# Kernel optimization log

Measured on AMD Instinct MI355X. Metric: run time of the kernel, lower is better.

## Reference

```python
import jax, jax.numpy as jnp
import numpy as np

D_MODEL = 1024
D_STATE = 16
D_CONV = 3
EXPAND = 2
MLP_RATIO = 4
HEADDIM = 64
D_INNER = EXPAND * D_MODEL            # 2048
NHEADS = D_INNER // HEADDIM           # 32
CONV_DIM = D_INNER + 2 * D_STATE      # x, B, C all go through the depthwise conv
D_IN_PROJ = 2 * D_INNER + 2 * D_STATE + NHEADS


def rmsnorm(x, w, eps=1e-6):
    return x * jax.lax.rsqrt(jnp.mean(x * x, axis=-1, keepdims=True) + eps) * w


def silu(x):
    return x * jax.nn.sigmoid(x)


def causal_depthwise_conv(x, w, b):
    # x: (B, L, C); w: (C, K); b: (C,)  -- causal depthwise conv over L
    B, L, C = x.shape
    K = w.shape[1]
    xp = jnp.pad(x, ((0, 0), (K - 1, 0), (0, 0)))
    out = b
    for k in range(K):  # tiny fixed loop over kernel taps (K=3)
        out = out + w[:, k] * xp[:, k:k + L, :]
    return out


def mamba2(h, W_in, conv_w, conv_b, dt_bias, A_log, D, norm_gate_w, W_out):
    B, L, _ = h.shape
    zxbcdt = h @ W_in  # (B, L, D_IN_PROJ)
    z = zxbcdt[..., :D_INNER]
    xBC = zxbcdt[..., D_INNER:D_INNER + CONV_DIM]
    dt = jax.nn.softplus(zxbcdt[..., D_INNER + CONV_DIM:] + dt_bias)  # (B, L, H)

    xBC = silu(causal_depthwise_conv(xBC, conv_w, conv_b))
    x = xBC[..., :D_INNER].reshape(B, L, NHEADS, HEADDIM)
    Bmat = xBC[..., D_INNER:D_INNER + D_STATE]   # (B, L, N)
    Cmat = xBC[..., D_INNER + D_STATE:]          # (B, L, N)

    A = -jnp.exp(A_log)                          # (H,)
    dA = jnp.exp(dt * A)                         # (B, L, H)
    dBx = jnp.einsum('blhp,bln,blh->blhpn', x, Bmat, dt)  # (B, L, H, P, N)

    def step(state, inp):
        dA_t, dBx_t = inp                        # (B,H), (B,H,P,N)
        state = state * dA_t[:, :, None, None] + dBx_t
        return state, state

    s0 = jnp.zeros((B, NHEADS, HEADDIM, D_STATE), dtype=h.dtype)
    _, states = jax.lax.scan(step, s0,
                             (jnp.moveaxis(dA, 1, 0), jnp.moveaxis(dBx, 1, 0)))
    # states: (L, B, H, P, N)
    y = jnp.einsum('lbhpn,bln->blhp', states, Cmat)
    y = y + D[None, None, :, None] * x
    y = y.reshape(B, L, D_INNER)
    y = rmsnorm(y * silu(z), norm_gate_w, eps=1e-5)  # gated RMSNorm as in Mamba2
    return y @ W_out


def setup_inputs() -> dict:
    key = jax.random.key(0)
    ks = jax.random.split(key, 12)
    f = jnp.float32
    d = {}
    d['x'] = jax.random.normal(ks[0], (2, 2048, D_MODEL), dtype=f)
    d['norm1_w'] = jnp.ones((D_MODEL,), f)
    d['W_in'] = jax.random.normal(ks[1], (D_MODEL, D_IN_PROJ), f) * (D_MODEL ** -0.5)
    d['conv_w'] = jax.random.normal(ks[2], (CONV_DIM, D_CONV), f) * 0.2
    d['conv_b'] = jnp.zeros((CONV_DIM,), f)
    d['dt_bias'] = jnp.log(jnp.expm1(jax.random.uniform(ks[3], (NHEADS,), f, 0.001, 0.1)))
    d['A_log'] = jnp.log(jax.random.uniform(ks[4], (NHEADS,), f, 1.0, 16.0))
    d['D'] = jnp.ones((NHEADS,), f)
    d['norm_gate_w'] = jnp.ones((D_INNER,), f)
    d['W_out'] = jax.random.normal(ks[5], (D_INNER, D_MODEL), f) * (D_INNER ** -0.5)
    d['norm2_w'] = jnp.ones((D_MODEL,), f)
    d['mlp_w1'] = jax.random.normal(ks[6], (D_MODEL, D_MODEL * MLP_RATIO), f) * (D_MODEL ** -0.5)
    d['mlp_b1'] = jnp.zeros((D_MODEL * MLP_RATIO,), f)
    d['mlp_w2'] = jax.random.normal(ks[7], (D_MODEL * MLP_RATIO, D_MODEL), f) * ((D_MODEL * MLP_RATIO) ** -0.5)
    d['mlp_b2'] = jnp.zeros((D_MODEL,), f)
    return d


def reference(x, norm1_w, W_in, conv_w, conv_b, dt_bias, A_log, D,
              norm_gate_w, W_out, norm2_w, mlp_w1, mlp_b1, mlp_w2, mlp_b2):
    h = rmsnorm(x, norm1_w)
    h = mamba2(h, W_in, conv_w, conv_b, dt_bias, A_log, D, norm_gate_w, W_out)
    x = x + h
    h = rmsnorm(x, norm2_w)
    h = silu(h @ mlp_w1 + mlp_b1) @ mlp_w2 + mlp_b2
    return x + h
```

## Files before the change

kernel.cpp:

```cpp
#include <hip/hip_runtime.h>

typedef __bf16 bf16;
typedef __bf16 bf16x4 __attribute__((ext_vector_type(4)));
typedef __bf16 bf16x8 __attribute__((ext_vector_type(8)));
typedef float  f32x4  __attribute__((ext_vector_type(4)));

#define BATCH  2
#define SEQ    2048
#define ROWS   (BATCH*SEQ)
#define DMODEL 1024
#define DINNER 2048
#define DSTATE 16
#define NH     32
#define HD     64
#define CONVD  2080
#define DPROJ  4160
#define DMLP   4096
#define DTOFF  (DINNER + CONVD)
#define CS     64
#define NCHUNK (SEQ/CS)

__device__ __forceinline__ float sigmoidf_(float x) { return 1.f / (1.f + expf(-x)); }

__device__ __forceinline__ float blockSum256(float v) {
    #pragma unroll
    for (int o = 32; o > 0; o >>= 1) v += __shfl_down(v, o);
    __shared__ float sb[4];
    const int tid = threadIdx.x;
    if ((tid & 63) == 0) sb[tid >> 6] = v;
    __syncthreads();
    return sb[0] + sb[1] + sb[2] + sb[3];
}

__device__ __forceinline__ void gload_lds16(const bf16* g, bf16* l) {
    __builtin_amdgcn_global_load_lds((const __attribute__((address_space(1))) void*)g,
                                     (__attribute__((address_space(3))) void*)l, 16, 0, 0);
}

__device__ __forceinline__ int xcd_swz(int orig, int nwg) {
    const int q = nwg >> 3, r = nwg & 7;
    const int x = orig & 7, i = orig >> 3;
    return (x < r ? x * (q + 1) : r * (q + 1) + (x - r) * q) + i;
}

__global__ __launch_bounds__(256) void transpose_k(const float* __restrict__ in,
                                                   bf16* __restrict__ out, int R, int C) {
    __shared__ float t[32][33];
    const int bx = blockIdx.x * 32, by = blockIdx.y * 32;
    const int tx = threadIdx.x, ty = threadIdx.y;
    #pragma unroll
    for (int i = 0; i < 4; ++i)
        t[ty + i * 8][tx] = in[(size_t)(by + ty + i * 8) * C + bx + tx];
    __syncthreads();
    #pragma unroll
    for (int i = 0; i < 4; ++i)
        out[(size_t)(bx + ty + i * 8) * R + by + tx] = (bf16)t[tx][ty + i * 8];
}

template<int EPI>
__global__ __launch_bounds__(512) void gemm256_k(
    const bf16* __restrict__ A, const bf16* __restrict__ BT,
    int K, int ldN, int colofs, int nbx, int nby,
    bf16* __restrict__ outb, float* __restrict__ outf,
    const float* __restrict__ bias, size_t pstride)
{
    __shared__ __align__(16) bf16 As[2][256 * 64];
    __shared__ __align__(16) bf16 Bs[2][256 * 64];
    const int nwg = (int)gridDim.x;
    const int wg  = xcd_swz((int)blockIdx.x, nwg);
    const int bx  = wg % nbx;
    const int t2  = wg / nbx;
    const int by  = t2 % nby;
    const int sl  = t2 / nby;
    const int ns  = nwg / (nbx * nby);
    const int Ks  = K / ns;
    const int kbeg = sl * Ks;

    const int tid  = threadIdx.x;
    const int lane = tid & 63, wid = tid >> 6;
    const int wm = wid >> 2, wn = wid & 3;
    const int lr = lane & 15, lk = lane >> 4;
    const int X  = lr & 7;
    const int brow = by * 256, bcol = bx * 256;

    size_t aoff[4], boff[4];
    #pragma unroll
    for (int i = 0; i < 4; ++i) {
        const int g = tid + i * 512;
        const int srow = g >> 3;
        const int scol = ((g & 7) ^ (srow & 7)) * 8;
        aoff[i] = (size_t)(brow + srow) * K + scol;
        boff[i] = (size_t)(bcol + srow) * K + scol;
    }

    auto stage = [&](int buf, int k0) {
        #pragma unroll
        for (int i = 0; i < 4; ++i)
            gload_lds16(A + aoff[i] + k0, As[buf] + (tid + i * 512) * 8);
        #pragma unroll
        for (int i = 0; i < 4; ++i)
            gload_lds16(BT + boff[i] + k0, Bs[buf] + (tid + i * 512) * 8);
    };

    f32x4 acc[8][4] = {};
    const int nt = Ks >> 6;
    stage(0, kbeg);
    __syncthreads();
    for (int t = 0; t < nt; ++t) {
        const int cur = t & 1;
        if (t + 1 < nt) stage(cur ^ 1, kbeg + (t + 1) * 64);
        #pragma unroll
        for (int kk = 0; kk < 2; ++kk) {
            const int off = ((kk * 4 + lk) ^ X) * 8;
            bf16x8 bfr[4];
            #pragma unroll
            for (int n = 0; n < 4; ++n)
                bfr[n] = *(const bf16x8*)(Bs[cur] + (wn * 64 + n * 16 + lr) * 64 + off);
            #pragma unroll
            for (int m = 0; m < 8; ++m) {
                const bf16x8 af = *(const bf16x8*)(As[cur] + (wm * 128 + m * 16 + lr) * 64 + off);
                #pragma unroll
                for (int n = 0; n < 4; ++n)
                    acc[m][n] = __builtin_amdgcn_mfma_f32_16x16x32_bf16(af, bfr[n], acc[m][n], 0, 0, 0);
            }
        }
        __syncthreads();
    }

    #pragma unroll
    for (int m = 0; m < 8; ++m) {
        const int grow = brow + wm * 128 + m * 16 + lk * 4;
        #pragma unroll
        for (int n = 0; n < 4; ++n) {
            const int gcol = colofs + bcol + wn * 64 + n * 16 + lr;
            #pragma unroll
            for (int j = 0; j < 4; ++j) {
                const int row = grow + j;
                float v = acc[m][n][j];
                if constexpr (EPI == 0) {
                    outb[(size_t)row * ldN + gcol] = (bf16)v;
                } else if constexpr (EPI == 1) {
                    v += bias[gcol];
                    outb[(size_t)row * ldN + gcol] = (bf16)(v * sigmoidf_(v));
                } else {
                    outf[pstride * sl + (size_t)row * ldN + gcol] = v;
                }
            }
        }
    }
}

template<int EPI>
__global__ __launch_bounds__(256) void gemm_bt(
    const bf16* __restrict__ A, const bf16* __restrict__ BT,
    int M, int N, int K, int nbx, int nby, int ldN, int colofs,
    bf16* __restrict__ outb, float* __restrict__ dtout)
{
    __shared__ __align__(16) bf16 As[2][128 * 64];
    __shared__ __align__(16) bf16 Bs[2][128 * 64];
    const int nwg = (int)gridDim.x;
    const int wg  = xcd_swz((int)blockIdx.x, nwg);
    const int bx  = wg % nbx;
    const int by  = (wg / nbx) % nby;

    const int tid  = threadIdx.x;
    const int brow = by * 128;
    const int bcol = bx * 128;
    const int lane = tid & 63;
    const int wid  = tid >> 6;
    const int wm = wid >> 1, wn = wid & 1;
    const int lr = lane & 15, lk = lane >> 4;
    const int X  = lr & 7;
    const int off0 = ((lk) ^ X) * 8;
    const int off1 = ((4 + lk) ^ X) * 8;

    f32x4 acc[4][4] = {};

    size_t aoff[4], boff[4];
    #pragma unroll
    for (int i = 0; i < 4; ++i) {
        const int g = tid + i * 256;
        const int srow = g >> 3;
        const int scol = ((g & 7) ^ (srow & 7)) * 8;
        aoff[i] = (size_t)(brow + srow) * K + scol;
        int bn = bcol + srow; if (bn > N - 1) bn = N - 1;
        boff[i] = (size_t)bn * K + scol;
    }

    auto stage = [&](int buf, int k0) {
        #pragma unroll
        for (int i = 0; i < 4; ++i)
            gload_lds16(A + aoff[i] + k0, As[buf] + (tid + i * 256) * 8);
        #pragma unroll
        for (int i = 0; i < 4; ++i)
            gload_lds16(BT + boff[i] + k0, Bs[buf] + (tid + i * 256) * 8);
    };

    const int nt = K >> 6;
    stage(0, 0);
    __syncthreads();
    for (int t = 0; t < nt; ++t) {
        const int cur = t & 1;
        if (t + 1 < nt) stage(cur ^ 1, (t + 1) * 64);
        #pragma unroll
        for (int kk = 0; kk < 2; ++kk) {
            const int off = kk ? off1 : off0;
            bf16x8 af[4], bfr[4];
            #pragma unroll
            for (int m = 0; m < 4; ++m)
                af[m] = *(const bf16x8*)(As[cur] + (wm * 64 + m * 16 + lr) * 64 + off);
            #pragma unroll
            for (int n = 0; n < 4; ++n)
                bfr[n] = *(const bf16x8*)(Bs[cur] + (wn * 64 + n * 16 + lr) * 64 + off);
            #pragma unroll
            for (int m = 0; m < 4; ++m)
                #pragma unroll
                for (int n = 0; n < 4; ++n)
                    acc[m][n] = __builtin_amdgcn_mfma_f32_16x16x32_bf16(af[m], bfr[n], acc[m][n], 0, 0, 0);
        }
        __syncthreads();
    }

    #pragma unroll
    for (int m = 0; m < 4; ++m) {
        const int grow = brow + wm * 64 + m * 16 + lk * 4;
        #pragma unroll
        for (int n = 0; n < 4; ++n) {
            const int gcol = bcol + wn * 64 + n * 16 + lr;
            if (gcol >= N) continue;
            #pragma unroll
            for (int j = 0; j < 4; ++j) {
                const int row = grow + j;
                const float v = acc[m][n][j];
                const int gc = colofs + gcol;
                outb[(size_t)row * ldN + gc] = (bf16)v;
                if (gc >= DTOFF)
                    dtout[(size_t)row * NH + (gc - DTOFF)] = v;
            }
        }
    }
}

template<int WITH_BIAS>
__global__ __launch_bounds__(256) void reduce_k(const float* __restrict__ part,
                                                const float* __restrict__ res,
                                                const float* __restrict__ bias,
                                                float* __restrict__ out, int MN) {
    const int i = (blockIdx.x * 256 + threadIdx.x) * 4;
    if (i >= MN) return;
    const float4 a = *(const float4*)(part + i);
    const float4 b = *(const float4*)(part + (size_t)MN + i);
    const float4 c = *(const float4*)(part + 2 * (size_t)MN + i);
    const float4 d = *(const float4*)(part + 3 * (size_t)MN + i);
    const float4 r = *(const float4*)(res + i);
    float4 o;
    o.x = a.x + b.x + c.x + d.x + r.x;
    o.y = a.y + b.y + c.y + d.y + r.y;
    o.z = a.z + b.z + c.z + d.z + r.z;
    o.w = a.w + b.w + c.w + d.w + r.w;
    if constexpr (WITH_BIAS) {
        const int col = i & (DMODEL - 1);
        o.x += bias[col]; o.y += bias[col + 1]; o.z += bias[col + 2]; o.w += bias[col + 3];
    }
    *(float4*)(out + i) = o;
}

__global__ __launch_bounds__(256) void rmsnorm_k(const float* __restrict__ in,
                                                 const float* __restrict__ w,
                                                 bf16* __restrict__ out, float eps) {
    const int row = blockIdx.x, tid = threadIdx.x;
    const float4 v = *(const float4*)(in + (size_t)row * DMODEL + tid * 4);
    float f[4] = { v.x, v.y, v.z, v.w };
    float ss = f[0]*f[0] + f[1]*f[1] + f[2]*f[2] + f[3]*f[3];
    ss = blockSum256(ss);
    const float scale = rsqrtf(ss * (1.f / DMODEL) + eps);
    const float4 wv = *(const float4*)(w + tid * 4);
    const float wa[4] = { wv.x, wv.y, wv.z, wv.w };
    bf16x4 o;
    #pragma unroll
    for (int j = 0; j < 4; ++j) o[j] = (bf16)(f[j] * scale * wa[j]);
    *(bf16x4*)(out + (size_t)row * DMODEL + tid * 4) = o;
}

__global__ __launch_bounds__(256) void rmsgate_k(const float* __restrict__ y,
                                                 const bf16* __restrict__ zx,
                                                 const float* __restrict__ w,
                                                 bf16* __restrict__ out) {
    const int row = blockIdx.x, tid = threadIdx.x;
    const float* yr = y + (size_t)row * DINNER;
    const bf16*  zr = zx + (size_t)row * DPROJ;
    float vals[8];
    float ss = 0.f;
    #pragma unroll
    for (int i = 0; i < 2; ++i) {
        const float4 yv = *(const float4*)(yr + tid * 8 + i * 4);
        const bf16x4 zv = *(const bf16x4*)(zr + tid * 8 + i * 4);
        const float ya[4] = { yv.x, yv.y, yv.z, yv.w };
        #pragma unroll
        for (int j = 0; j < 4; ++j) {
            const float z = (float)zv[j];
            const float t = ya[j] * (z * sigmoidf_(z));
            vals[i * 4 + j] = t;
            ss += t * t;
        }
    }
    ss = blockSum256(ss);
    const float scale = rsqrtf(ss * (1.f / DINNER) + 1e-5f);
    bf16* orow = out + (size_t)row * DINNER + tid * 8;
    #pragma unroll
    for (int i = 0; i < 2; ++i) {
        bf16x4 o;
        #pragma unroll
        for (int j = 0; j < 4; ++j)
            o[j] = (bf16)(vals[i * 4 + j] * scale * w[tid * 8 + i * 4 + j]);
        *(bf16x4*)(orow + i * 4) = o;
    }
}

__global__ __launch_bounds__(256) void conv_silu_k(const bf16* __restrict__ zx,
                                                   const float* __restrict__ cw,
                                                   const float* __restrict__ cb,
                                                   float* __restrict__ xBC) {
    const int idx = blockIdx.x * 256 + threadIdx.x;
    if (idx >= ROWS * CONVD) return;
    const int c  = idx % CONVD;
    const int bl = idx / CONVD;
    const int l  = bl % SEQ;
    float acc = cb[c];
    const bf16* col = zx + (size_t)bl * DPROJ + DINNER + c;
    if (l >= 2) acc += cw[c * 3 + 0] * (float)col[-2 * DPROJ];
    if (l >= 1) acc += cw[c * 3 + 1] * (float)col[-1 * DPROJ];
    acc += cw[c * 3 + 2] * (float)col[0];
    acc = acc * sigmoidf_(acc);
    xBC[(size_t)bl * CONVD + c] = acc;
}

__global__ __launch_bounds__(256) void dtda_k(const float* __restrict__ dtraw,
                                              const float* __restrict__ dt_bias,
                                              const float* __restrict__ A_log,
                                              float* __restrict__ dtb,
                                              float* __restrict__ dab) {
    const int idx = blockIdx.x * 256 + threadIdx.x;
    if (idx >= ROWS * NH) return;
    const int h = idx & (NH - 1);
    const float raw = dtraw[idx] + dt_bias[h];
    const float dt = raw > 20.f ? raw : log1pf(expf(raw));
    const float dA = expf(-expf(A_log[h]) * dt);
    dtb[idx] = dt;
    dab[idx] = dA;
}

__global__ __launch_bounds__(256) void scan1_k(const float* __restrict__ xBC,
                                               const float* __restrict__ dtb,
                                               const float* __restrict__ dab,
                                               float* __restrict__ Sloc,
                                               float* __restrict__ Pc) {
    const int c = blockIdx.x & (NCHUNK - 1);
    const int h = (blockIdx.x >> 5) & (NH - 1);
    const int b = blockIdx.x >> 10;
    const int tid = threadIdx.x;
    const int p  = tid >> 2;
    const int nq = (tid & 3) * 4;
    const size_t rb = (size_t)b * SEQ + c * CS;
    const float* xrow = xBC + rb * CONVD + h * HD + p;
    const float* Brow = xBC + rb * CONVD + DINNER + nq;
    const float* dtp = dtb + rb * NH + h;
    const float* dap = dab + rb * NH + h;
    float s0 = 0.f, s1 = 0.f, s2 = 0.f, s3 = 0.f, P = 1.f;
    for (int l = 0; l < CS; ++l) {
        const float xv  = xrow[(size_t)l * CONVD];
        const float4 Bv = *(const float4*)(Brow + (size_t)l * CONVD);
        const float dtv = dtp[l * NH];
        const float dav = dap[l * NH];
        const float xdt = xv * dtv;
        s0 = s0 * dav + xdt * Bv.x;
        s1 = s1 * dav + xdt * Bv.y;
        s2 = s2 * dav + xdt * Bv.z;
        s3 = s3 * dav + xdt * Bv.w;
        P *= dav;
    }
    float4* dst = (float4*)(Sloc + (size_t)blockIdx.x * 1024 + tid * 4);
    *dst = make_float4(s0, s1, s2, s3);
    if (tid == 0) Pc[blockIdx.x] = P;
}

__global__ __launch_bounds__(256) void scan2_k(const float* __restrict__ Sloc,
                                               const float* __restrict__ Pc,
                                               float* __restrict__ Sini) {
    const int bh = blockIdx.x;
    const int tid = threadIdx.x;
    const size_t base = (size_t)bh * NCHUNK;
    float c0 = 0.f, c1 = 0.f, c2 = 0.f, c3 = 0.f;
    for (int c = 0; c < NCHUNK; ++c) {
        *(float4*)(Sini + (base + c) * 1024 + tid * 4) = make_float4(c0, c1, c2, c3);
        const float4 sl = *(const float4*)(Sloc + (base + c) * 1024 + tid * 4);
        const float P = Pc[base + c];
        c0 = c0 * P + sl.x;
        c1 = c1 * P + sl.y;
        c2 = c2 * P + sl.z;
        c3 = c3 * P + sl.w;
    }
}

__global__ __launch_bounds__(256) void scan3_k(const float* __restrict__ xBC,
                                               const float* __restrict__ dtb,
                                               const float* __restrict__ dab,
                                               const float* __restrict__ Dp,
                                               const float* __restrict__ Sini,
                                               float* __restrict__ y) {
    const int c = blockIdx.x & (NCHUNK - 1);
    const int h = (blockIdx.x >> 5) & (NH - 1);
    const int b = blockIdx.x >> 10;
    const int tid = threadIdx.x;
    const int p  = tid >> 2;
    const int nq = (tid & 3) * 4;
    const float Dh = Dp[h];
    const size_t rb = (size_t)b * SEQ + c * CS;
    const float* xrow = xBC + rb * CONVD + h * HD + p;
    const float* Brow = xBC + rb * CONVD + DINNER + nq;
    const float* Crow = xBC + rb * CONVD + DINNER + DSTATE + nq;
    const float* dtp = dtb + rb * NH + h;
    const float* dap = dab + rb * NH + h;
    float* yp = y + rb * DINNER + h * HD + p;
    const float4 si = *(const float4*)(Sini + (size_t)blockIdx.x * 1024 + tid * 4);
    float s0 = si.x, s1 = si.y, s2 = si.z, s3 = si.w;
    for (int l = 0; l < CS; ++l) {
        const float xv  = xrow[(size_t)l * CONVD];
        const float4 Bv = *(const float4*)(Brow + (size_t)l * CONVD);
        const float4 Cv = *(const float4*)(Crow + (size_t)l * CONVD);
        const float dtv = dtp[l * NH];
        const float dav = dap[l * NH];
        const float xdt = xv * dtv;
        s0 = s0 * dav + xdt * Bv.x;
        s1 = s1 * dav + xdt * Bv.y;
        s2 = s2 * dav + xdt * Bv.z;
        s3 = s3 * dav + xdt * Bv.w;
        float part = s0 * Cv.x + s1 * Cv.y + s2 * Cv.z + s3 * Cv.w;
        part += __shfl_xor(part, 1);
        part += __shfl_xor(part, 2);
        if ((tid & 3) == 0) yp[(size_t)l * DINNER] = part + Dh * xv;
    }
}

extern "C" void kernel_launch(void* const* d_in, const int* in_sizes, int n_in,
                              void* d_out, int out_size, void* d_ws, size_t ws_size,
                              hipStream_t stream) {
    const float* x       = (const float*)d_in[0];
    const float* n1w     = (const float*)d_in[1];
    const float* W_in    = (const float*)d_in[2];
    const float* conv_w  = (const float*)d_in[3];
    const float* conv_b  = (const float*)d_in[4];
    const float* dt_bias = (const float*)d_in[5];
    const float* A_log   = (const float*)d_in[6];
    const float* Dp      = (const float*)d_in[7];
    const float* ngw     = (const float*)d_in[8];
    const float* W_out   = (const float*)d_in[9];
    const float* n2w     = (const float*)d_in[10];
    const float* w1      = (const float*)d_in[11];
    const float* b1      = (const float*)d_in[12];
    const float* w2      = (const float*)d_in[13];
    const float* b2      = (const float*)d_in[14];
    float* out = (float*)d_out;

    char* p = (char*)d_ws;
    auto alloc = [&](size_t bytes) -> char* {
        char* q = p;
        p += (bytes + 255) & ~(size_t)255;
        return q;
    };
    bf16*  W_inT  = (bf16*) alloc((size_t)DPROJ  * DMODEL * 2);
    bf16*  W_outT = (bf16*) alloc((size_t)DMODEL * DINNER * 2);
    bf16*  w1T    = (bf16*) alloc((size_t)DMLP   * DMODEL * 2);
    bf16*  w2T    = (bf16*) alloc((size_t)DMODEL * DMLP   * 2);
    bf16*  h1     = (bf16*) alloc((size_t)ROWS * DMODEL * 2);
    bf16*  zx     = (bf16*) alloc((size_t)ROWS * DPROJ  * 2);
    float* dtraw  = (float*)alloc((size_t)ROWS * NH * 4);
    float* xBC    = (float*)alloc((size_t)ROWS * CONVD * 4);
    float* dtb    = (float*)alloc((size_t)ROWS * NH * 4);
    float* dab    = (float*)alloc((size_t)ROWS * NH * 4);
    float* ybuf   = (float*)alloc((size_t)ROWS * DINNER * 4);
    bf16*  ynorm  = (bf16*) alloc((size_t)ROWS * DINNER * 2);
    float* x2     = (float*)alloc((size_t)ROWS * DMODEL * 4);
    bf16*  h2     = (bf16*) alloc((size_t)ROWS * DMODEL * 2);
    bf16*  mid    = (bf16*) alloc((size_t)ROWS * DMLP * 2);
    float* Sloc   = (float*)alloc((size_t)BATCH * NH * NCHUNK * 1024 * 4);
    float* Sini   = (float*)alloc((size_t)BATCH * NH * NCHUNK * 1024 * 4);
    float* Pc     = (float*)alloc((size_t)BATCH * NH * NCHUNK * 4);
    float* part   = (float*)zx;
    const size_t pstride = (size_t)ROWS * DMODEL;
    (void)ws_size; (void)in_sizes; (void)n_in; (void)out_size;

    const dim3 tb(32, 8);
    transpose_k<<<dim3(DPROJ / 32, DMODEL / 32), tb, 0, stream>>>(W_in, W_inT, DMODEL, DPROJ);
    transpose_k<<<dim3(DMODEL / 32, DINNER / 32), tb, 0, stream>>>(W_out, W_outT, DINNER, DMODEL);
    transpose_k<<<dim3(DMLP / 32, DMODEL / 32), tb, 0, stream>>>(w1, w1T, DMODEL, DMLP);
    transpose_k<<<dim3(DMODEL / 32, DMLP / 32), tb, 0, stream>>>(w2, w2T, DMLP, DMODEL);

    rmsnorm_k<<<ROWS, 256, 0, stream>>>(x, n1w, h1, 1e-6f);

    gemm_bt<0><<<32, 256, 0, stream>>>(
        h1, W_inT + (size_t)4096 * DMODEL, ROWS, 64, DMODEL, 1, 32, DPROJ, 4096, zx, dtraw);
    gemm256_k<0><<<256, 512, 0, stream>>>(
        h1, W_inT, DMODEL, DPROJ, 0, 16, 16, zx, nullptr, nullptr, 0);

    conv_silu_k<<<(ROWS * CONVD + 255) / 256, 256, 0, stream>>>(zx, conv_w, conv_b, xBC);
    dtda_k<<<(ROWS * NH + 255) / 256, 256, 0, stream>>>(dtraw, dt_bias, A_log, dtb, dab);

    scan1_k<<<BATCH * NH * NCHUNK, 256, 0, stream>>>(xBC, dtb, dab, Sloc, Pc);
    scan2_k<<<BATCH * NH, 256, 0, stream>>>(Sloc, Pc, Sini);
    scan3_k<<<BATCH * NH * NCHUNK, 256, 0, stream>>>(xBC, dtb, dab, Dp, Sini, ybuf);

    rmsgate_k<<<ROWS, 256, 0, stream>>>(ybuf, zx, ngw, ynorm);

    gemm256_k<2><<<4 * 16 * 4, 512, 0, stream>>>(
        ynorm, W_outT, DINNER, DMODEL, 0, 4, 16, nullptr, part, nullptr, pstride);
    reduce_k<0><<<(ROWS * DMODEL / 4 + 255) / 256, 256, 0, stream>>>(
        part, x, nullptr, x2, ROWS * DMODEL);

    rmsnorm_k<<<ROWS, 256, 0, stream>>>(x2, n2w, h2, 1e-6f);

    gemm256_k<1><<<16 * 16, 512, 0, stream>>>(
        h2, w1T, DMODEL, DMLP, 0, 16, 16, mid, nullptr, b1, 0);

    gemm256_k<2><<<4 * 16 * 4, 512, 0, stream>>>(
        mid, w2T, DMLP, DMODEL, 0, 4, 16, nullptr, part, nullptr, pstride);
    reduce_k<1><<<(ROWS * DMODEL / 4 + 255) / 256, 256, 0, stream>>>(
        part, x2, b2, out, ROWS * DMODEL);
}
```

Measured before the change: 354.5 us.

## Merge in-projection GEMMs into one launch and fuse split-K reduce with RMSNorm

Replaces the two-launch input projection (large-tile GEMM plus a small tail GEMM for dt columns) with a single 128x128-tile GEMM over all projection columns that also writes the dt slice. Fuses the split-K partial reduction and residual add after the output projection with the second RMSNorm, so x2 is not re-read. This removes launches and a full-tensor pass, but gives up the larger tile's data reuse for the main in-projection GEMM.

Measured after the change: 345.4 us. 1.03x faster.

```diff
diff --git a/kernel.cpp b/kernel.cpp
--- a/kernel.cpp
+++ b/kernel.cpp
@@ -57,10 +57,99 @@
         out[(size_t)(bx + ty + i * 8) * R + by + tx] = (bf16)t[tx][ty + i * 8];
 }
 
+__global__ __launch_bounds__(256) void gemm_bt(
+    const bf16* __restrict__ A, const bf16* __restrict__ BT,
+    int M, int N, int K, int nbx, int nby,
+    bf16* __restrict__ outb, float* __restrict__ dtout)
+{
+    __shared__ __align__(16) bf16 As[2][128 * 64];
+    __shared__ __align__(16) bf16 Bs[2][128 * 64];
+    const int nwg = (int)gridDim.x;
+    const int wg  = xcd_swz((int)blockIdx.x, nwg);
+    const int bx  = wg % nbx;
+    const int by  = (wg / nbx) % nby;
+
+    const int tid  = threadIdx.x;
+    const int brow = by * 128;
+    const int bcol = bx * 128;
+    const int lane = tid & 63;
+    const int wid  = tid >> 6;
+    const int wm = wid >> 1, wn = wid & 1;
+    const int lr = lane & 15, lk = lane >> 4;
+    const int X  = lr & 7;
+    const int off0 = ((lk) ^ X) * 8;
+    const int off1 = ((4 + lk) ^ X) * 8;
+
+    f32x4 acc[4][4] = {};
+
+    size_t aoff[4], boff[4];
+    #pragma unroll
+    for (int i = 0; i < 4; ++i) {
+        const int g = tid + i * 256;
+        const int srow = g >> 3;
+        const int scol = ((g & 7) ^ (srow & 7)) * 8;
+        aoff[i] = (size_t)(brow + srow) * K + scol;
+        int bn = bcol + srow; if (bn > N - 1) bn = N - 1;
+        boff[i] = (size_t)bn * K + scol;
+    }
+
+    auto stage = [&](int buf, int k0) {
+        #pragma unroll
+        for (int i = 0; i < 4; ++i)
+            gload_lds16(A + aoff[i] + k0, As[buf] + (tid + i * 256) * 8);
+        #pragma unroll
+        for (int i = 0; i < 4; ++i)
+            gload_lds16(BT + boff[i] + k0, Bs[buf] + (tid + i * 256) * 8);
+    };
+
+    const int nt = K >> 6;
+    stage(0, 0);
+    __syncthreads();
+    for (int t = 0; t < nt; ++t) {
+        const int cur = t & 1;
+        if (t + 1 < nt) stage(cur ^ 1, (t + 1) * 64);
+        #pragma unroll
+        for (int kk = 0; kk < 2; ++kk) {
+            const int off = kk ? off1 : off0;
+            bf16x8 af[4], bfr[4];
+            #pragma unroll
+            for (int m = 0; m < 4; ++m)
+                af[m] = *(const bf16x8*)(As[cur] + (wm * 64 + m * 16 + lr) * 64 + off);
+            #pragma unroll
+            for (int n = 0; n < 4; ++n)
+                bfr[n] = *(const bf16x8*)(Bs[cur] + (wn * 64 + n * 16 + lr) * 64 + off);
+            #pragma unroll
+            for (int m = 0; m < 4; ++m)
+                #pragma unroll
+                for (int n = 0; n < 4; ++n)
+                    acc[m][n] = __builtin_amdgcn_mfma_f32_16x16x32_bf16(af[m], bfr[n], acc[m][n], 0, 0, 0);
+        }
+        __syncthreads();
+    }
+
+    #pragma unroll
+    for (int m = 0; m < 4; ++m) {
+        const int grow = brow + wm * 64 + m * 16 + lk * 4;
+        #pragma unroll
+        for (int n = 0; n < 4; ++n) {
+            const int gcol = bcol + wn * 64 + n * 16 + lr;
+            if (gcol >= N) continue;
+            #pragma unroll
+            for (int j = 0; j < 4; ++j) {
+                const int row = grow + j;
+                const float v = acc[m][n][j];
+                outb[(size_t)row * N + gcol] = (bf16)v;
+                if (gcol >= DTOFF)
+                    dtout[(size_t)row * NH + (gcol - DTOFF)] = v;
+            }
+        }
+    }
+}
+
 template<int EPI>
 __global__ __launch_bounds__(512) void gemm256_k(
     const bf16* __restrict__ A, const bf16* __restrict__ BT,
-    int K, int ldN, int colofs, int nbx, int nby,
+    int K, int ldN, int nbx, int nby,
     bf16* __restrict__ outb, float* __restrict__ outf,
     const float* __restrict__ bias, size_t pstride)
 {
@@ -132,14 +221,12 @@
         const int grow = brow + wm * 128 + m * 16 + lk * 4;
         #pragma unroll
         for (int n = 0; n < 4; ++n) {
-            const int gcol = colofs + bcol + wn * 64 + n * 16 + lr;
+            const int gcol = bcol + wn * 64 + n * 16 + lr;
             #pragma unroll
             for (int j = 0; j < 4; ++j) {
                 const int row = grow + j;
                 float v = acc[m][n][j];
-                if constexpr (EPI == 0) {
-                    outb[(size_t)row * ldN + gcol] = (bf16)v;
-                } else if constexpr (EPI == 1) {
+                if constexpr (EPI == 1) {
                     v += bias[gcol];
                     outb[(size_t)row * ldN + gcol] = (bf16)(v * sigmoidf_(v));
                 } else {
@@ -150,98 +237,36 @@
     }
 }
 
-template<int EPI>
-__global__ __launch_bounds__(256) void gemm_bt(
-    const bf16* __restrict__ A, const bf16* __restrict__ BT,
-    int M, int N, int K, int nbx, int nby, int ldN, int colofs,
-    bf16* __restrict__ outb, float* __restrict__ dtout)
-{
-    __shared__ __align__(16) bf16 As[2][128 * 64];
-    __shared__ __align__(16) bf16 Bs[2][128 * 64];
-    const int nwg = (int)gridDim.x;
-    const int wg  = xcd_swz((int)blockIdx.x, nwg);
-    const int bx  = wg % nbx;
-    const int by  = (wg / nbx) % nby;
-
-    const int tid  = threadIdx.x;
-    const int brow = by * 128;
-    const int bcol = bx * 128;
-    const int lane = tid & 63;
-    const int wid  = tid >> 6;
-    const int wm = wid >> 1, wn = wid & 1;
-    const int lr = lane & 15, lk = lane >> 4;
-    const int X  = lr & 7;
-    const int off0 = ((lk) ^ X) * 8;
-    const int off1 = ((4 + lk) ^ X) * 8;
-
-    f32x4 acc[4][4] = {};
-
-    size_t aoff[4], boff[4];
-    #pragma unroll
-    for (int i = 0; i < 4; ++i) {
-        const int g = tid + i * 256;
-        const int srow = g >> 3;
-        const int scol = ((g & 7) ^ (srow & 7)) * 8;
-        aoff[i] = (size_t)(brow + srow) * K + scol;
-        int bn = bcol + srow; if (bn > N - 1) bn = N - 1;
-        boff[i] = (size_t)bn * K + scol;
-    }
-
-    auto stage = [&](int buf, int k0) {
-        #pragma unroll
-        for (int i = 0; i < 4; ++i)
-            gload_lds16(A + aoff[i] + k0, As[buf] + (tid + i * 256) * 8);
-        #pragma unroll
-        for (int i = 0; i < 4; ++i)
-            gload_lds16(BT + boff[i] + k0, Bs[buf] + (tid + i * 256) * 8);
-    };
-
-    const int nt = K >> 6;
-    stage(0, 0);
-    __syncthreads();
-    for (int t = 0; t < nt; ++t) {
-        const int cur = t & 1;
-        if (t + 1 < nt) stage(cur ^ 1, (t + 1) * 64);
-        #pragma unroll
-        for (int kk = 0; kk < 2; ++kk) {
-            const int off = kk ? off1 : off0;
-            bf16x8 af[4], bfr[4];
-            #pragma unroll
-            for (int m = 0; m < 4; ++m)
-                af[m] = *(const bf16x8*)(As[cur] + (wm * 64 + m * 16 + lr) * 64 + off);
-            #pragma unroll
-            for (int n = 0; n < 4; ++n)
-                bfr[n] = *(const bf16x8*)(Bs[cur] + (wn * 64 + n * 16 + lr) * 64 + off);
-            #pragma unroll
-            for (int m = 0; m < 4; ++m)
-                #pragma unroll
-                for (int n = 0; n < 4; ++n)
-                    acc[m][n] = __builtin_amdgcn_mfma_f32_16x16x32_bf16(af[m], bfr[n], acc[m][n], 0, 0, 0);
-        }
-        __syncthreads();
-    }
-
-    #pragma unroll
-    for (int m = 0; m < 4; ++m) {
-        const int grow = brow + wm * 64 + m * 16 + lk * 4;
-        #pragma unroll
-        for (int n = 0; n < 4; ++n) {
-            const int gcol = bcol + wn * 64 + n * 16 + lr;
-            if (gcol >= N) continue;
-            #pragma unroll
-            for (int j = 0; j < 4; ++j) {
-                const int row = grow + j;
-                const float v = acc[m][n][j];
-                const int gc = colofs + gcol;
-                outb[(size_t)row * ldN + gc] = (bf16)v;
-                if (gc >= DTOFF)
-                    dtout[(size_t)row * NH + (gc - DTOFF)] = v;
-            }
-        }
-    }
-}
-
-template<int WITH_BIAS>
+__global__ __launch_bounds__(256) void reduce_norm_k(const float* __restrict__ part,
+                                                     const float* __restrict__ res,
+                                                     const float* __restrict__ w,
+                                                     float* __restrict__ x2,
+                                                     bf16* __restrict__ h2) {
+    const int row = blockIdx.x, tid = threadIdx.x;
+    const size_t MN = (size_t)ROWS * DMODEL;
+    const size_t i = (size_t)row * DMODEL + tid * 4;
+    const float4 a = *(const float4*)(part + i);
+    const float4 b = *(const float4*)(part + MN + i);
+    const float4 c = *(const float4*)(part + 2 * MN + i);
+    const float4 d = *(const float4*)(part + 3 * MN + i);
+    const float4 r = *(const float4*)(res + i);
+    float f[4];
+    f[0] = a.x + b.x + c.x + d.x + r.x;
+    f[1] = a.y + b.y + c.y + d.y + r.y;
+    f[2] = a.z + b.z + c.z + d.z + r.z;
+    f[3] = a.w + b.w + c.w + d.w + r.w;
+    *(float4*)(x2 + i) = make_float4(f[0], f[1], f[2], f[3]);
+    float ss = f[0]*f[0] + f[1]*f[1] + f[2]*f[2] + f[3]*f[3];
+    ss = blockSum256(ss);
+    const float scale = rsqrtf(ss * (1.f / DMODEL) + 1e-6f);
+    const float4 wv = *(const float4*)(w + tid * 4);
+    const float wa[4] = { wv.x, wv.y, wv.z, wv.w };
+    bf16x4 o;
+    #pragma unroll
+    for (int j = 0; j < 4; ++j) o[j] = (bf16)(f[j] * scale * wa[j]);
+    *(bf16x4*)(h2 + i) = o;
+}
+
 __global__ __launch_bounds__(256) void reduce_k(const float* __restrict__ part,
                                                 const float* __restrict__ res,
                                                 const float* __restrict__ bias,
@@ -253,15 +278,12 @@
     const float4 c = *(const float4*)(part + 2 * (size_t)MN + i);
     const float4 d = *(const float4*)(part + 3 * (size_t)MN + i);
     const float4 r = *(const float4*)(res + i);
+    const int col = i & (DMODEL - 1);
     float4 o;
-    o.x = a.x + b.x + c.x + d.x + r.x;
-    o.y = a.y + b.y + c.y + d.y + r.y;
-    o.z = a.z + b.z + c.z + d.z + r.z;
-    o.w = a.w + b.w + c.w + d.w + r.w;
-    if constexpr (WITH_BIAS) {
-        const int col = i & (DMODEL - 1);
-        o.x += bias[col]; o.y += bias[col + 1]; o.z += bias[col + 2]; o.w += bias[col + 3];
-    }
+    o.x = a.x + b.x + c.x + d.x + r.x + bias[col];
+    o.y = a.y + b.y + c.y + d.y + r.y + bias[col + 1];
+    o.z = a.z + b.z + c.z + d.z + r.z + bias[col + 2];
+    o.w = a.w + b.w + c.w + d.w + r.w + bias[col + 3];
     *(float4*)(out + i) = o;
 }
 
@@ -498,10 +520,8 @@
 
     rmsnorm_k<<<ROWS, 256, 0, stream>>>(x, n1w, h1, 1e-6f);
 
-    gemm_bt<0><<<32, 256, 0, stream>>>(
-        h1, W_inT + (size_t)4096 * DMODEL, ROWS, 64, DMODEL, 1, 32, DPROJ, 4096, zx, dtraw);
-    gemm256_k<0><<<256, 512, 0, stream>>>(
-        h1, W_inT, DMODEL, DPROJ, 0, 16, 16, zx, nullptr, nullptr, 0);
+    gemm_bt<<<33 * 32, 256, 0, stream>>>(
+        h1, W_inT, ROWS, DPROJ, DMODEL, 33, 32, zx, dtraw);
 
     conv_silu_k<<<(ROWS * CONVD + 255) / 256, 256, 0, stream>>>(zx, conv_w, conv_b, xBC);
     dtda_k<<<(ROWS * NH + 255) / 256, 256, 0, stream>>>(dtraw, dt_bias, A_log, dtb, dab);
@@ -513,17 +533,14 @@
     rmsgate_k<<<ROWS, 256, 0, stream>>>(ybuf, zx, ngw, ynorm);
 
     gemm256_k<2><<<4 * 16 * 4, 512, 0, stream>>>(
-        ynorm, W_outT, DINNER, DMODEL, 0, 4, 16, nullptr, part, nullptr, pstride);
-    reduce_k<0><<<(ROWS * DMODEL / 4 + 255) / 256, 256, 0, stream>>>(
-        part, x, nullptr, x2, ROWS * DMODEL);
-
-    rmsnorm_k<<<ROWS, 256, 0, stream>>>(x2, n2w, h2, 1e-6f);
+        ynorm, W_outT, DINNER, DMODEL, 4, 16, nullptr, part, nullptr, pstride);
+    reduce_norm_k<<<ROWS, 256, 0, stream>>>(part, x, n2w, x2, h2);
 
     gemm256_k<1><<<16 * 16, 512, 0, stream>>>(
-        h2, w1T, DMODEL, DMLP, 0, 16, 16, mid, nullptr, b1, 0);
+        h2, w1T, DMODEL, DMLP, 16, 16, mid, nullptr, b1, 0);
 
     gemm256_k<2><<<4 * 16 * 4, 512, 0, stream>>>(
-        mid, w2T, DMLP, DMODEL, 0, 4, 16, nullptr, part, nullptr, pstride);
-    reduce_k<1><<<(ROWS * DMODEL / 4 + 255) / 256, 256, 0, stream>>>(
+        mid, w2T, DMLP, DMODEL, 4, 16, nullptr, part, nullptr, pstride);
+    reduce_k<<<(ROWS * DMODEL / 4 + 255) / 256, 256, 0, stream>>>(
         part, x2, b2, out, ROWS * DMODEL);
 }
```
